# Optimization experiments

Measured on AMD Instinct MI355X. Metric: run time of the kernel, lower is better.

The kernel has to match this reference:

```python
import jax, jax.numpy as jnp
import numpy as np

N_SRC, M, K, H = 100000, 20000, 32, 128
NEG_SLOPE = 0.01  # torch LeakyReLU default


def setup_inputs() -> dict:
    key = jax.random.key(0)
    ks = jax.random.split(key, 8)
    nei = jax.random.randint(ks[0], (M, K), 0, N_SRC)
    h = jax.random.normal(ks[1], (N_SRC, 1), dtype=jnp.float32)
    h_refer = jax.random.normal(ks[2], (M, 1), dtype=jnp.float32)
    # map_l / map_r: Linear(1, H), weight init U[0,1), bias U[0,0.01)
    map_l_w = jax.random.uniform(ks[3], (H, 1), dtype=jnp.float32)
    map_l_b = jax.random.uniform(ks[4], (H,), dtype=jnp.float32) * 0.01
    map_r_w = jax.random.uniform(ks[5], (H, 1), dtype=jnp.float32)
    map_r_b = jax.random.uniform(ks[6], (H,), dtype=jnp.float32) * 0.01
    # att_inter: xavier_normal gain=1.414 on shape (1, 2H)
    std = 1.414 * np.sqrt(2.0 / (1 + 2 * H))
    att_inter = jax.random.normal(ks[7], (1, 2 * H), dtype=jnp.float32) * std
    return {"nei": nei, "h": h, "h_refer": h_refer,
            "map_l_w": map_l_w, "map_l_b": map_l_b,
            "map_r_w": map_r_w, "map_r_b": map_r_b,
            "att_inter": att_inter}


def reference(nei, h, h_refer, map_l_w, map_l_b, map_r_w, map_r_b, att_inter):
    # project scalar features to H dims
    h = jax.nn.relu(h @ map_l_w.T + map_l_b)            # [N, H]
    hr = jax.nn.relu(h_refer @ map_r_w.T + map_r_b)     # [M, H]
    nei_emb = h[nei]                                    # [M, K, H] gather
    # split attention vector to avoid materializing concat([hr, nei_emb])
    a_ref = att_inter[0, :H]                            # [H]
    a_nei = att_inter[0, H:]                            # [H]
    logits = (hr @ a_ref)[:, None] + nei_emb @ a_nei    # [M, K]
    logits = jnp.where(logits >= 0, logits, NEG_SLOPE * logits)  # leakyrelu
    att = jax.nn.softmax(logits, axis=1)                # softmax over neighbors
    lr_inner = jnp.einsum('mkh,mh->mk', nei_emb, hr)    # [M, K]
    out = jax.nn.relu(jnp.sum(att * lr_inner, axis=1, keepdims=True))  # [M, 1]
    return (out, att)
```

## Files before the change

kernel.cpp:

```cpp
#include <hip/hip_runtime.h>

#define N_SRC 100000
#define M_NODES 20000
#define K_NEI 32
#define H_DIM 128
#define NEG_SLOPE 0.01f

#define BLK_M 80
#define NTHR 640
#define SH_STRIDE 132

__global__ __launch_bounds__(NTHR) void intra_att_fused(
    const int*   __restrict__ nei,
    const float* __restrict__ h,
    const float* __restrict__ h_refer,
    const float* __restrict__ map_l_w,
    const float* __restrict__ map_l_b,
    const float* __restrict__ map_r_w,
    const float* __restrict__ map_r_b,
    const float* __restrict__ att_inter,
    float*       __restrict__ out,
    float*       __restrict__ att)
{
    __shared__ float  s_traw[H_DIM];
    __shared__ int    s_ord[H_DIM];
    __shared__ float  s_T[H_DIM + 8];
    __shared__ float  s_wr[H_DIM], s_br[H_DIM], s_ar[H_DIM];
    __shared__ float  s_wl[H_DIM], s_bl[H_DIM];
    __shared__ float  s_cw[H_DIM], s_cb[H_DIM];
    __shared__ float2 s_SA[H_DIM + 1];
    __shared__ float2 s_SH[BLK_M][SH_STRIDE];

    const int tid  = threadIdx.x;
    const int slot = tid >> 3;
    const int u    = tid & 7;
    const int m    = blockIdx.x * BLK_M + slot;

    const int4  nv = *(const int4*)(nei + m * K_NEI + u * 4);
    const float rm = h_refer[m];

    if (tid < H_DIM) {
        const float wl0 = map_l_w[tid];
        const float bl0 = map_l_b[tid];
        s_traw[tid] = -bl0 / fmaxf(wl0, 1e-30f);
    }
    const float x0 = h[nv.x], x1 = h[nv.y], x2 = h[nv.z], x3 = h[nv.w];
    __syncthreads();

    if (tid < H_DIM) {
        const float t0 = s_traw[tid];
        int rank = 0;
        #pragma unroll 8
        for (int i = 0; i < H_DIM; ++i) {
            const float ti = s_traw[i];
            rank += (ti < t0 || (ti == t0 && i < tid)) ? 1 : 0;
        }
        s_ord[rank] = tid;
    }
    __syncthreads();

    if (tid < H_DIM) {
        const int   src = s_ord[tid];
        const float wls = map_l_w[src];
        const float bls = map_l_b[src];
        const float an  = att_inter[H_DIM + src];
        s_T[tid]  = s_traw[src];
        s_wl[tid] = wls;
        s_bl[tid] = bls;
        s_wr[tid] = map_r_w[src];
        s_br[tid] = map_r_b[src];
        s_ar[tid] = att_inter[src];
        s_cw[tid] = an * wls;
        s_cb[tid] = an * bls;
    } else if (tid < H_DIM + 8) {
        s_T[tid] = 3.4e38f;
    }
    __syncthreads();

    if (tid < 8) {
        const int sb0 = tid * 16;
        float cwv[16], cbv[16];
        float sw = 0.f, sbv = 0.f;
        #pragma unroll
        for (int i = 0; i < 16; ++i) {
            cwv[i] = s_cw[sb0 + i]; cbv[i] = s_cb[sb0 + i];
            sw += cwv[i]; sbv += cbv[i];
        }
        float iw = sw, ib = sbv, v;
        v = __shfl_up(iw, 1); if (tid >= 1) iw += v;
        v = __shfl_up(ib, 1); if (tid >= 1) ib += v;
        v = __shfl_up(iw, 2); if (tid >= 2) iw += v;
        v = __shfl_up(ib, 2); if (tid >= 2) ib += v;
        v = __shfl_up(iw, 4); if (tid >= 4) iw += v;
        v = __shfl_up(ib, 4); if (tid >= 4) ib += v;
        float rw = iw - sw, rb = ib - sbv;
        #pragma unroll
        for (int i = 0; i < 16; ++i) {
            s_SA[sb0 + i] = make_float2(rw, rb);
            rw += cwv[i]; rb += cbv[i];
        }
        if (tid == 7) s_SA[H_DIM] = make_float2(rw, rb);
    }

    float Tm[16];
    #pragma unroll
    for (int i = 0; i < 16; ++i) Tm[i] = s_T[i * 8 + 7];

    const int sb = u * 16;
    float hrdot = 0.f;
    float cw[16], cb[16];
    float sw = 0.f, sbv = 0.f;
    #pragma unroll
    for (int q = 0; q < 4; ++q) {
        const float4 wr4 = *(const float4*)(s_wr + sb + q * 4);
        const float4 br4 = *(const float4*)(s_br + sb + q * 4);
        const float4 ar4 = *(const float4*)(s_ar + sb + q * 4);
        const float4 wl4 = *(const float4*)(s_wl + sb + q * 4);
        const float4 bl4 = *(const float4*)(s_bl + sb + q * 4);
        const float h0 = fmaxf(0.f, fmaf(rm, wr4.x, br4.x));
        const float h1 = fmaxf(0.f, fmaf(rm, wr4.y, br4.y));
        const float h2 = fmaxf(0.f, fmaf(rm, wr4.z, br4.z));
        const float h3 = fmaxf(0.f, fmaf(rm, wr4.w, br4.w));
        hrdot += h0*ar4.x + h1*ar4.y + h2*ar4.z + h3*ar4.w;
        cw[q*4+0] = h0*wl4.x; cb[q*4+0] = h0*bl4.x;
        cw[q*4+1] = h1*wl4.y; cb[q*4+1] = h1*bl4.y;
        cw[q*4+2] = h2*wl4.z; cb[q*4+2] = h2*bl4.z;
        cw[q*4+3] = h3*wl4.w; cb[q*4+3] = h3*bl4.w;
        sw  += cw[q*4+0] + cw[q*4+1] + cw[q*4+2] + cw[q*4+3];
        sbv += cb[q*4+0] + cb[q*4+1] + cb[q*4+2] + cb[q*4+3];
    }
    {
        float iw = sw, ib = sbv, v;
        v = __shfl_up(iw, 1); if (u >= 1) iw += v;
        v = __shfl_up(ib, 1); if (u >= 1) ib += v;
        v = __shfl_up(iw, 2); if (u >= 2) iw += v;
        v = __shfl_up(ib, 2); if (u >= 2) ib += v;
        v = __shfl_up(iw, 4); if (u >= 4) iw += v;
        v = __shfl_up(ib, 4); if (u >= 4) ib += v;
        float rw = iw - sw, rb = ib - sbv;
        #pragma unroll
        for (int q = 0; q < 8; ++q) {
            float4 t4;
            t4.x = rw; t4.y = rb; rw += cw[q*2];   rb += cb[q*2];
            t4.z = rw; t4.w = rb; rw += cw[q*2+1]; rb += cb[q*2+1];
            *(float4*)(&s_SH[slot][sb + q*2]) = t4;
        }
        if (u == 7) s_SH[slot][H_DIM] = make_float2(rw, rb);
    }
    hrdot += __shfl_xor(hrdot, 1);
    hrdot += __shfl_xor(hrdot, 2);
    hrdot += __shfl_xor(hrdot, 4);

    __syncthreads();

    const float xs[4] = {x0, x1, x2, x3};
    float lg[4], in_[4];
    float mx = -3.4e38f;
    #pragma unroll
    for (int t = 0; t < 4; ++t) {
        const float x = xs[t];
        int r = 0;
        #pragma unroll
        for (int i = 0; i < 16; ++i) r += (Tm[i] < x) ? 8 : 0;
        if (s_T[r + 3] < x) r += 4;
        if (s_T[r + 1] < x) r += 2;
        if (s_T[r]     < x) r += 1;
        const float2 sa = s_SA[r];
        const float2 sh = s_SH[slot][r];
        const float l = fmaf(sa.x, x, sa.y) + hrdot;
        lg[t]  = (l >= 0.f) ? l : NEG_SLOPE * l;
        in_[t] = fmaf(sh.x, x, sh.y);
        mx = fmaxf(mx, lg[t]);
    }
    mx = fmaxf(mx, __shfl_xor(mx, 1));
    mx = fmaxf(mx, __shfl_xor(mx, 2));
    mx = fmaxf(mx, __shfl_xor(mx, 4));

    float e[4];
    float se = 0.f, sei = 0.f;
    #pragma unroll
    for (int t = 0; t < 4; ++t) {
        e[t] = __expf(lg[t] - mx);
        se  += e[t];
        sei += e[t] * in_[t];
    }
    se  += __shfl_xor(se, 1);  se  += __shfl_xor(se, 2);  se  += __shfl_xor(se, 4);
    sei += __shfl_xor(sei, 1); sei += __shfl_xor(sei, 2); sei += __shfl_xor(sei, 4);

    const float inv = 1.0f / se;
    const float4 a4 = make_float4(e[0]*inv, e[1]*inv, e[2]*inv, e[3]*inv);
    *(float4*)(att + m * K_NEI + u * 4) = a4;
    if (u == 0) out[m] = fmaxf(0.f, sei * inv);
}

extern "C" void kernel_launch(void* const* d_in, const int* in_sizes, int n_in,
                              void* d_out, int out_size, void* d_ws, size_t ws_size,
                              hipStream_t stream) {
    const int*   nei       = (const int*)  d_in[0];
    const float* h         = (const float*)d_in[1];
    const float* h_refer   = (const float*)d_in[2];
    const float* map_l_w   = (const float*)d_in[3];
    const float* map_l_b   = (const float*)d_in[4];
    const float* map_r_w   = (const float*)d_in[5];
    const float* map_r_b   = (const float*)d_in[6];
    const float* att_inter = (const float*)d_in[7];

    float* out = (float*)d_out;
    float* att = out + M_NODES;

    const int blocks = M_NODES / BLK_M;
    intra_att_fused<<<blocks, NTHR, 0, stream>>>(
        nei, h, h_refer, map_l_w, map_l_b, map_r_w, map_r_b, att_inter,
        out, att);
}
```

Measured before the change: 17.61 us.

## Shrink blocks to 128 threads and vectorise rank and bucket searches

Blocks drop from 80 to 16 rows (640 to 128 threads), so the launch grows from 250 to 1250 blocks and every thread takes part in the per-block threshold sort without branching. The rank loop now reads thresholds as float4, and the bucket search replaces a 3-step binary search with two float4 loads and a count of eight compares. The cost is that each block still redoes the 128-element O(H^2) sort and parameter setup, and with five times as many blocks that fixed work is repeated five times as often.

```diff
diff --git a/kernel.cpp b/kernel.cpp
--- a/kernel.cpp
+++ b/kernel.cpp
@@ -6,11 +6,10 @@
 #define H_DIM 128
 #define NEG_SLOPE 0.01f
 
-#define BLK_M 80
-#define NTHR 640
+#define BLK_M 16
 #define SH_STRIDE 132
 
-__global__ __launch_bounds__(NTHR) void intra_att_fused(
+__global__ __launch_bounds__(128) void intra_att_fused(
     const int*   __restrict__ nei,
     const float* __restrict__ h,
     const float* __restrict__ h_refer,
@@ -22,9 +21,9 @@
     float*       __restrict__ out,
     float*       __restrict__ att)
 {
-    __shared__ float  s_traw[H_DIM];
+    __shared__ __attribute__((aligned(16))) float  s_traw[H_DIM];
     __shared__ int    s_ord[H_DIM];
-    __shared__ float  s_T[H_DIM + 8];
+    __shared__ __attribute__((aligned(16))) float  s_T[H_DIM + 8];
     __shared__ float  s_wr[H_DIM], s_br[H_DIM], s_ar[H_DIM];
     __shared__ float  s_wl[H_DIM], s_bl[H_DIM];
     __shared__ float  s_cw[H_DIM], s_cb[H_DIM];
@@ -39,27 +38,29 @@
     const int4  nv = *(const int4*)(nei + m * K_NEI + u * 4);
     const float rm = h_refer[m];
 
-    if (tid < H_DIM) {
-        const float wl0 = map_l_w[tid];
-        const float bl0 = map_l_b[tid];
-        s_traw[tid] = -bl0 / fmaxf(wl0, 1e-30f);
-    }
+    const float wl0 = map_l_w[tid];
+    const float bl0 = map_l_b[tid];
+    const float t0  = -bl0 / fmaxf(wl0, 1e-30f);
+    s_traw[tid] = t0;
+
     const float x0 = h[nv.x], x1 = h[nv.y], x2 = h[nv.z], x3 = h[nv.w];
-    __syncthreads();
-
-    if (tid < H_DIM) {
-        const float t0 = s_traw[tid];
-        int rank = 0;
-        #pragma unroll 8
-        for (int i = 0; i < H_DIM; ++i) {
-            const float ti = s_traw[i];
-            rank += (ti < t0 || (ti == t0 && i < tid)) ? 1 : 0;
-        }
-        s_ord[rank] = tid;
-    }
-    __syncthreads();
-
-    if (tid < H_DIM) {
+
+    __syncthreads();
+
+    int rank = 0;
+    #pragma unroll 8
+    for (int q = 0; q < H_DIM / 4; ++q) {
+        const float4 tq = *(const float4*)(s_traw + q * 4);
+        const int b = q * 4;
+        rank += (tq.x < t0 || (tq.x == t0 && (b + 0) < tid)) ? 1 : 0;
+        rank += (tq.y < t0 || (tq.y == t0 && (b + 1) < tid)) ? 1 : 0;
+        rank += (tq.z < t0 || (tq.z == t0 && (b + 2) < tid)) ? 1 : 0;
+        rank += (tq.w < t0 || (tq.w == t0 && (b + 3) < tid)) ? 1 : 0;
+    }
+    s_ord[rank] = tid;
+    __syncthreads();
+
+    {
         const int   src = s_ord[tid];
         const float wls = map_l_w[src];
         const float bls = map_l_b[src];
@@ -72,8 +73,7 @@
         s_ar[tid] = att_inter[src];
         s_cw[tid] = an * wls;
         s_cb[tid] = an * bls;
-    } else if (tid < H_DIM + 8) {
-        s_T[tid] = 3.4e38f;
+        if (tid < 8) s_T[H_DIM + tid] = 3.4e38f;
     }
     __syncthreads();
 
@@ -162,9 +162,10 @@
         int r = 0;
         #pragma unroll
         for (int i = 0; i < 16; ++i) r += (Tm[i] < x) ? 8 : 0;
-        if (s_T[r + 3] < x) r += 4;
-        if (s_T[r + 1] < x) r += 2;
-        if (s_T[r]     < x) r += 1;
+        const float4 ta = *(const float4*)(s_T + r);
+        const float4 tb = *(const float4*)(s_T + r + 4);
+        r += (ta.x < x) + (ta.y < x) + (ta.z < x) + (ta.w < x)
+           + (tb.x < x) + (tb.y < x) + (tb.z < x) + (tb.w < x);
         const float2 sa = s_SA[r];
         const float2 sh = s_SH[slot][r];
         const float l = fmaf(sa.x, x, sa.y) + hrdot;
@@ -209,7 +210,7 @@
     float* att = out + M_NODES;
 
     const int blocks = M_NODES / BLK_M;
-    intra_att_fused<<<blocks, NTHR, 0, stream>>>(
+    intra_att_fused<<<blocks, 128, 0, stream>>>(
         nei, h, h_refer, map_l_w, map_l_b, map_r_w, map_r_b, att_inter,
         out, att);
 }
```

Result: slower. 18.95 us (+7.6%).
